# Performance work log

Measured on AMD Instinct MI355X. Metric: run time of the kernel, lower is better.

## Reference

```python
import jax, jax.numpy as jnp
import numpy as np

N, K, D = 32768, 1024, 256
TAU = 1.0          # gumbel-softmax temperature (torch default)
KL_WEIGHT = 1.0    # settings.kl_weight stand-in
EPS = 1e-6


def setup_inputs() -> dict:
    key = jax.random.key(0)
    k1, k2, k3 = jax.random.split(key, 3)
    latents = jax.random.normal(k1, (N, D), dtype=jnp.float32)
    # torch init: uniform_(-1/num_protos, 1/num_protos)
    prototypes = jax.random.uniform(k2, (K, D), dtype=jnp.float32,
                                    minval=-1.0 / K, maxval=1.0 / K)
    u = jax.random.uniform(k3, (N, K), dtype=jnp.float32,
                           minval=1e-10, maxval=1.0)
    gumbel = -jnp.log(-jnp.log(u))  # Gumbel(0,1) noise
    return {"latents": latents, "prototypes": prototypes, "gumbel": gumbel}


def reference(latents, prototypes, gumbel):
    # squared euclidean distances latents[:,None,:] - prototypes -> [N, K]
    # expanded form (same math, avoids [N,K,D] intermediate):
    d2 = (jnp.sum(latents * latents, axis=-1, keepdims=True)
          - 2.0 * latents @ prototypes.T
          + jnp.sum(prototypes * prototypes, axis=-1))
    logits = (-d2 + gumbel) / TAU
    logprobs = jax.nn.log_softmax(logits, axis=-1)      # [N, K]
    y_soft = jnp.exp(logprobs)
    # hard=True straight-through one-hot
    idx = jnp.argmax(y_soft, axis=-1)
    y_hard = jax.nn.one_hot(idx, K, dtype=y_soft.dtype)
    onehot = y_hard - jax.lax.stop_gradient(y_soft) + y_soft
    quantized = onehot @ prototypes                     # [N, D]

    # prior over codes (batch mean of probs), broadcast to all rows
    prior = jnp.mean(y_soft + EPS, axis=0)              # [K]
    # KLDivLoss(reduction='batchmean')(logprobs, prior):
    # mean over rows of sum_k prior_k * (log prior_k - logprobs_k)
    capacity = jnp.mean(jnp.sum(prior * (jnp.log(prior) - logprobs), axis=-1))
    ent = -jnp.sum(prior * jnp.log(prior))
    # settings.epoch <= 5000 branch: subtract entropy term
    vq_loss = KL_WEIGHT * capacity - 0.001 * ent
    return quantized, vq_loss
```

## Files before the change

### kernel.cpp

```cpp
#include <hip/hip_runtime.h>
#include <hip/hip_bf16.h>
#include <stdint.h>

#define NN 32768
#define KK 1024
#define DD 256
#define BM 16
#define CHUNK 128
#define NCHUNK (KK / CHUNK)
#define NTHR 512
#define NRB (NN / BM)

#define LXS 0
#define LPS 8192
#define ASC_MAXP 73728
#define ASC_ZP   74752
#define ASC_MI   75264
#define LA_TOT   75328

#define LSS 8192
#define LRM (LSS + 32768)
#define LRI (LRM + 64)
#define FLPS 41216
#define LTOT_PRE  41216
#define LTOT_NPRE (41216 + 65536)

#define PB_OFF   12288
#define SBUF_OFF 536576
#define LZ_OFF   (SBUF_OFF + (size_t)NRB * NCHUNK * 512 * 8)
#define WS_FULL  (LZ_OFF + (size_t)NN * 4)
#define WS_PRE   (PB_OFF + (size_t)KK * DD * 2)

typedef __attribute__((ext_vector_type(8))) short bf16x8;
typedef __attribute__((ext_vector_type(4))) float f32x4;

__device__ __forceinline__ uint32_t pkbf2(float a, float b) {
    uint32_t ua = __builtin_bit_cast(uint32_t, a);
    uint32_t ub = __builtin_bit_cast(uint32_t, b);
    ua = (ua + 0x7fffu + ((ua >> 16) & 1u)) >> 16;
    ub = (ub + 0x7fffu + ((ub >> 16) & 1u)) >> 16;
    return ua | (ub << 16);
}
__device__ __forceinline__ float ubf(uint32_t h) {
    return __builtin_bit_cast(float, h << 16);
}

__global__ void vq_init(const float* __restrict__ protos, float* __restrict__ ws) {
    int k = blockIdx.x * 256 + threadIdx.x;
    const float4* p4 = reinterpret_cast<const float4*>(protos + (size_t)k * DD);
    float s = 0.f;
#pragma unroll 8
    for (int j = 0; j < DD / 4; ++j) {
        float4 v = p4[j];
        s = fmaf(v.x, v.x, s); s = fmaf(v.y, v.y, s);
        s = fmaf(v.z, v.z, s); s = fmaf(v.w, v.w, s);
    }
    ws[k] = s;
    ws[KK + k] = 0.f;
    ws[2 * KK + k] = 0.f;
}

__global__ void vq_cvt(const float* __restrict__ protos, uint32_t* __restrict__ pb) {
    int idx = blockIdx.x * 256 + threadIdx.x;
    const float4* s = reinterpret_cast<const float4*>(protos + (size_t)idx * 8);
    float4 a = s[0], b = s[1];
    uint4 v;
    v.x = pkbf2(a.x, a.y); v.y = pkbf2(a.z, a.w);
    v.z = pkbf2(b.x, b.y); v.w = pkbf2(b.z, b.w);
    reinterpret_cast<uint4*>(pb)[idx] = v;
}

__global__ __launch_bounds__(NTHR) void vq_mainA(const float* __restrict__ latents,
                                                 const float* __restrict__ protos,
                                                 const float* __restrict__ gumbel,
                                                 float* __restrict__ ws,
                                                 float* __restrict__ out) {
    __shared__ __align__(16) unsigned char sm[LA_TOT];
    const int t = threadIdx.x;
    const int lane = t & 63;
    const int w = t >> 6;
    const int rb = blockIdx.x;
    const int n0 = rb * BM;
    const int l15 = lane & 15;
    const int l4 = lane >> 4;
    const float* np2 = ws;
    const uint4* pb = reinterpret_cast<const uint4*>((char*)ws + PB_OFF);
    uint2* Sb = reinterpret_cast<uint2*>((char*)ws + SBUF_OFF);
    float* lzb = reinterpret_cast<float*>((char*)ws + LZ_OFF);

    {
        int row = t >> 5, g = t & 31;
        const float4* src = reinterpret_cast<const float4*>(
            latents + (size_t)(n0 + row) * DD + g * 8);
        float4 a = src[0], b = src[1];
        uint4 v; v.x = pkbf2(a.x, a.y); v.y = pkbf2(a.z, a.w);
        v.z = pkbf2(b.x, b.y); v.w = pkbf2(b.z, b.w);
        *reinterpret_cast<uint4*>(sm + LXS + row * 512 + ((g ^ (row & 7)) << 4)) = v;
    }

    const int pr = w * 16 + l15;
    const int cwbase = w * 16 + l4 * 4;
    float z = 0.f, m = -3.4e38f; int mi = 0;

    for (int c = 0; c < NCHUNK; ++c) {
        __syncthreads();
#pragma unroll
        for (int i = 0; i < 8; ++i) {
            int G = t + NTHR * i;
            int p = G >> 5, g = G & 31;
            *reinterpret_cast<uint4*>(sm + LPS + p * 512 + ((g ^ (p & 7)) << 4)) =
                pb[(size_t)(c * CHUNK + p) * 32 + g];
        }
        __syncthreads();

        const int pg0 = c * CHUNK + cwbase;
        float4 q4 = *reinterpret_cast<const float4*>(np2 + pg0);
        float4 g4 = *reinterpret_cast<const float4*>(gumbel + (size_t)(n0 + l15) * KK + pg0);

        f32x4 acc = {0.f, 0.f, 0.f, 0.f};
#pragma unroll
        for (int ks = 0; ks < 8; ++ks) {
            int gi = ks * 4 + l4;
            bf16x8 af = *reinterpret_cast<bf16x8*>(sm + LPS + pr * 512 + ((gi ^ (pr & 7)) << 4));
            bf16x8 b0 = *reinterpret_cast<bf16x8*>(sm + LXS + l15 * 512 + ((gi ^ (l15 & 7)) << 4));
            acc = __builtin_amdgcn_mfma_f32_16x16x32_bf16(af, b0, acc, 0, 0, 0);
        }
        float s0 = fmaf(2.f, acc.x, -q4.x) + g4.x;
        float s1 = fmaf(2.f, acc.y, -q4.y) + g4.y;
        float s2 = fmaf(2.f, acc.z, -q4.z) + g4.z;
        float s3 = fmaf(2.f, acc.w, -q4.w) + g4.w;
        z += __expf(s0) + __expf(s1) + __expf(s2) + __expf(s3);
        if (s0 > m) { m = s0; mi = pg0; }
        if (s1 > m) { m = s1; mi = pg0 + 1; }
        if (s2 > m) { m = s2; mi = pg0 + 2; }
        if (s3 > m) { m = s3; mi = pg0 + 3; }
        uint2 pk;
        pk.x = pkbf2(s0, s1);
        pk.y = pkbf2(s2, s3);
        Sb[((size_t)rb * NCHUNK + c) * 512 + t] = pk;
    }

#pragma unroll
    for (int off = 16; off <= 32; off <<= 1) {
        float om = __shfl_xor(m, off); int oi = __shfl_xor(mi, off);
        if (om > m || (om == m && oi < mi)) { m = om; mi = oi; }
        z += __shfl_xor(z, off);
    }
    if (lane < 16) {
        *reinterpret_cast<float*>(sm + ASC_MAXP + (l15 * 8 + w) * 8) = m;
        *reinterpret_cast<int*>(sm + ASC_MAXP + (l15 * 8 + w) * 8 + 4) = mi;
        *reinterpret_cast<float*>(sm + ASC_ZP + (l15 * 8 + w) * 4) = z;
    }
    __syncthreads();
    if (t < 16) {
        float mm = -3.4e38f; int mmi = 0; float Z = 0.f;
#pragma unroll
        for (int j = 0; j < 8; ++j) {
            float om = *reinterpret_cast<float*>(sm + ASC_MAXP + (t * 8 + j) * 8);
            int oi = *reinterpret_cast<int*>(sm + ASC_MAXP + (t * 8 + j) * 8 + 4);
            if (om > mm || (om == mm && oi < mmi)) { mm = om; mmi = oi; }
            Z += *reinterpret_cast<float*>(sm + ASC_ZP + (t * 8 + j) * 4);
        }
        lzb[n0 + t] = __logf(Z);
        *reinterpret_cast<int*>(sm + ASC_MI + t * 4) = mmi;
    }
    __syncthreads();

    {
        int row = t >> 5, v = t & 31;
        int idx = *reinterpret_cast<int*>(sm + ASC_MI + row * 4);
        const float4* src = reinterpret_cast<const float4*>(protos + (size_t)idx * DD + v * 8);
        float4* dst = reinterpret_cast<float4*>(out + (size_t)(n0 + row) * DD + v * 8);
        dst[0] = src[0];
        dst[1] = src[1];
    }
}

__global__ __launch_bounds__(NTHR) void vq_colsum(float* __restrict__ ws) {
    const int t = threadIdx.x;
    const int l15 = t & 15;
    const int c = blockIdx.x & 7;
    const int rg = blockIdx.x >> 3;
    const uint2* Sb = reinterpret_cast<const uint2*>((char*)ws + SBUF_OFF);
    const float* lzb = reinterpret_cast<const float*>((char*)ws + LZ_OFF);
    float* colsum_y = ws + KK;
    float* colsum_lp = ws + 2 * KK;

    float sy0 = 0.f, sy1 = 0.f, sy2 = 0.f, sy3 = 0.f;
    float sl0 = 0.f, sl1 = 0.f, sl2 = 0.f, sl3 = 0.f;
    for (int i = 0; i < NRB / 32; ++i) {
        int rb = rg * (NRB / 32) + i;
        uint2 v = Sb[((size_t)rb * NCHUNK + c) * 512 + t];
        float lz = lzb[rb * BM + l15];
        float a0 = ubf(v.x & 0xffffu) - lz, a1 = ubf(v.x >> 16) - lz;
        float a2 = ubf(v.y & 0xffffu) - lz, a3 = ubf(v.y >> 16) - lz;
        sy0 += __expf(a0); sy1 += __expf(a1); sy2 += __expf(a2); sy3 += __expf(a3);
        sl0 += a0; sl1 += a1; sl2 += a2; sl3 += a3;
    }
#pragma unroll
    for (int off = 1; off < 16; off <<= 1) {
        sy0 += __shfl_xor(sy0, off); sy1 += __shfl_xor(sy1, off);
        sy2 += __shfl_xor(sy2, off); sy3 += __shfl_xor(sy3, off);
        sl0 += __shfl_xor(sl0, off); sl1 += __shfl_xor(sl1, off);
        sl2 += __shfl_xor(sl2, off); sl3 += __shfl_xor(sl3, off);
    }
    if (l15 == 0) {
        int w = t >> 6, l4 = (t & 63) >> 4;
        int cb = c * CHUNK + w * 16 + l4 * 4;
        atomicAdd(&colsum_y[cb],     sy0); atomicAdd(&colsum_y[cb + 1], sy1);
        atomicAdd(&colsum_y[cb + 2], sy2); atomicAdd(&colsum_y[cb + 3], sy3);
        atomicAdd(&colsum_lp[cb],     sl0); atomicAdd(&colsum_lp[cb + 1], sl1);
        atomicAdd(&colsum_lp[cb + 2], sl2); atomicAdd(&colsum_lp[cb + 3], sl3);
    }
}

template<bool PRE>
__global__ __launch_bounds__(NTHR) void vq_mainT(const float* __restrict__ latents,
                                                 const float* __restrict__ protos,
                                                 const float* __restrict__ gumbel,
                                                 float* __restrict__ ws,
                                                 float* __restrict__ out) {
    __shared__ __align__(16) unsigned char sm[PRE ? LTOT_PRE : LTOT_NPRE];
    const int t = threadIdx.x;
    const int lane = t & 63;
    const int w = t >> 6;
    const int n0 = blockIdx.x * BM;
    const int l15 = lane & 15;
    const int l4 = lane >> 4;
    const float* np2 = ws;
    float* colsum_y = ws + KK;
    float* colsum_lp = ws + 2 * KK;
    const uint4* pb = reinterpret_cast<const uint4*>((char*)ws + PB_OFF);

    {
        int row = t >> 5, g = t & 31;
        const float4* src = reinterpret_cast<const float4*>(
            latents + (size_t)(n0 + row) * DD + g * 8);
        float4 a = src[0], b = src[1];
        uint4 v; v.x = pkbf2(a.x, a.y); v.y = pkbf2(a.z, a.w);
        v.z = pkbf2(b.x, b.y); v.w = pkbf2(b.z, b.w);
        *reinterpret_cast<uint4*>(sm + LXS + row * 512 + ((g ^ (row & 7)) << 4)) = v;
    }
    __syncthreads();

    const int pr = w * 16 + l15;
    const int cwbase = w * 16 + l4 * 4;

    for (int c = 0; c < NCHUNK; ++c) {
        if (!PRE) {
            __syncthreads();
#pragma unroll
            for (int i = 0; i < 8; ++i) {
                int G = t + NTHR * i;
                int p = G >> 5, g = G & 31;
                const float4* src = reinterpret_cast<const float4*>(
                    protos + (size_t)(c * CHUNK + p) * DD + g * 8);
                float4 a = src[0], b = src[1];
                uint4 v; v.x = pkbf2(a.x, a.y); v.y = pkbf2(a.z, a.w);
                v.z = pkbf2(b.x, b.y); v.w = pkbf2(b.z, b.w);
                *reinterpret_cast<uint4*>(sm + FLPS + p * 512 + ((g ^ (p & 7)) << 4)) = v;
            }
            __syncthreads();
        }
        const int pg0 = c * CHUNK + cwbase;
        float4 q4 = *reinterpret_cast<const float4*>(np2 + pg0);
        float4 g4 = *reinterpret_cast<const float4*>(gumbel + (size_t)(n0 + l15) * KK + pg0);

        f32x4 acc = {0.f, 0.f, 0.f, 0.f};
        if (PRE) {
            const uint4* afp = pb + (size_t)(c * CHUNK + pr) * 32;
#pragma unroll
            for (int ks = 0; ks < 8; ++ks) {
                int gi = ks * 4 + l4;
                bf16x8 af = __builtin_bit_cast(bf16x8, afp[gi]);
                bf16x8 b0 = *reinterpret_cast<bf16x8*>(
                    sm + LXS + l15 * 512 + ((gi ^ (l15 & 7)) << 4));
                acc = __builtin_amdgcn_mfma_f32_16x16x32_bf16(af, b0, acc, 0, 0, 0);
            }
        } else {
#pragma unroll
            for (int ks = 0; ks < 8; ++ks) {
                int gi = ks * 4 + l4;
                bf16x8 af = *reinterpret_cast<bf16x8*>(
                    sm + FLPS + pr * 512 + ((gi ^ (pr & 7)) << 4));
                bf16x8 b0 = *reinterpret_cast<bf16x8*>(
                    sm + LXS + l15 * 512 + ((gi ^ (l15 & 7)) << 4));
                acc = __builtin_amdgcn_mfma_f32_16x16x32_bf16(af, b0, acc, 0, 0, 0);
            }
        }
        {
            const int Gs = pg0 >> 2;
            uint2 pk;
            pk.x = pkbf2(fmaf(2.f, acc.x, -q4.x) + g4.x, fmaf(2.f, acc.y, -q4.y) + g4.y);
            pk.y = pkbf2(fmaf(2.f, acc.z, -q4.z) + g4.z, fmaf(2.f, acc.w, -q4.w) + g4.w);
            *reinterpret_cast<uint2*>(sm + LSS + l15 * 2048 + ((Gs ^ ((l15 & 7) << 1)) << 3)) = pk;
        }
    }
    __syncthreads();

    {
        int row = t >> 5, v = t & 31;
        int sw = (row & 7) << 1;
        uint2 d[8];
#pragma unroll
        for (int j = 0; j < 8; ++j) {
            int G = v + 32 * j;
            d[j] = *reinterpret_cast<uint2*>(sm + LSS + row * 2048 + ((G ^ sw) << 3));
        }
        float m = -3.4e38f; int mi = 0;
#pragma unroll
        for (int j = 0; j < 8; ++j) {
            int c0 = (v + 32 * j) * 4;
            float f0 = ubf(d[j].x & 0xffffu), f1 = ubf(d[j].x >> 16);
            float f2 = ubf(d[j].y & 0xffffu), f3 = ubf(d[j].y >> 16);
            if (f0 > m) { m = f0; mi = c0; }
            if (f1 > m) { m = f1; mi = c0 + 1; }
            if (f2 > m) { m = f2; mi = c0 + 2; }
            if (f3 > m) { m = f3; mi = c0 + 3; }
        }
#pragma unroll
        for (int off = 1; off < 32; off <<= 1) {
            float om = __shfl_xor(m, off);
            int oi = __shfl_xor(mi, off);
            if (om > m || (om == m && oi < mi)) { m = om; mi = oi; }
        }
        float se = 0.f;
#pragma unroll
        for (int j = 0; j < 8; ++j) {
            se += __expf(ubf(d[j].x & 0xffffu) - m);
            se += __expf(ubf(d[j].x >> 16) - m);
            se += __expf(ubf(d[j].y & 0xffffu) - m);
            se += __expf(ubf(d[j].y >> 16) - m);
        }
#pragma unroll
        for (int off = 1; off < 32; off <<= 1) se += __shfl_xor(se, off);
        if (v == 0) {
            *reinterpret_cast<float*>(sm + LRM + row * 4) = m + __logf(se);
            *reinterpret_cast<int*>(sm + LRI + row * 4) = mi;
        }
    }
    __syncthreads();

#pragma unroll
    for (int h = 0; h < 2; ++h) {
        int col = t + h * NTHR;
        int G = col >> 2;
        int e2 = (col & 3) << 1;
        float sy = 0.f, slp = 0.f;
#pragma unroll 8
        for (int r = 0; r < BM; ++r) {
            uint32_t hv = *reinterpret_cast<uint16_t*>(
                sm + LSS + r * 2048 + ((G ^ ((r & 7) << 1)) << 3) + e2);
            float lz = *reinterpret_cast<float*>(sm + LRM + r * 4);
            float lp = ubf(hv) - lz;
            slp += lp;
            sy += __expf(lp);
        }
        atomicAdd(&colsum_y[col], sy);
        atomicAdd(&colsum_lp[col], slp);
    }

    {
        int row = t >> 5, v = t & 31;
        int idx = *reinterpret_cast<int*>(sm + LRI + row * 4);
        const float4* src = reinterpret_cast<const float4*>(protos + (size_t)idx * DD + v * 8);
        float4* dst = reinterpret_cast<float4*>(out + (size_t)(n0 + row) * DD + v * 8);
        dst[0] = src[0];
        dst[1] = src[1];
    }
}

__global__ void vq_final(const float* __restrict__ ws,
                         float* __restrict__ out, int out_size) {
    __shared__ float part[4];
    int t = threadIdx.x;
    const float invN = 1.0f / (float)NN;
    float a = 0.f;
    for (int j = 0; j < 4; ++j) {
        int k = t + j * 256;
        float prior = fmaf(ws[KK + k], invN, 1e-6f);
        float Lk = ws[2 * KK + k] * invN;
        a += prior * (1.001f * __logf(prior) - Lk);
    }
#pragma unroll
    for (int off = 32; off >= 1; off >>= 1) a += __shfl_xor(a, off);
    if ((t & 63) == 0) part[t >> 6] = a;
    __syncthreads();
    if (t == 0) {
        out[out_size - 1] = part[0] + part[1] + part[2] + part[3];
    }
}

extern "C" void kernel_launch(void* const* d_in, const int* in_sizes, int n_in,
                              void* d_out, int out_size, void* d_ws, size_t ws_size,
                              hipStream_t stream) {
    (void)in_sizes; (void)n_in;
    const float* latents = (const float*)d_in[0];
    const float* protos  = (const float*)d_in[1];
    const float* gumbel  = (const float*)d_in[2];
    float* out           = (float*)d_out;
    float* ws            = (float*)d_ws;

    vq_init<<<dim3(4), dim3(256), 0, stream>>>(protos, ws);
    if (ws_size >= WS_FULL) {
        vq_cvt<<<dim3(KK * DD / 2048), dim3(256), 0, stream>>>(
            protos, (uint32_t*)((char*)d_ws + PB_OFF));
        vq_mainA<<<dim3(NRB), dim3(NTHR), 0, stream>>>(
            latents, protos, gumbel, ws, out);
        vq_colsum<<<dim3(NCHUNK * 32), dim3(NTHR), 0, stream>>>(ws);
    } else if (ws_size >= WS_PRE) {
        vq_cvt<<<dim3(KK * DD / 2048), dim3(256), 0, stream>>>(
            protos, (uint32_t*)((char*)d_ws + PB_OFF));
        vq_mainT<true><<<dim3(NRB), dim3(NTHR), 0, stream>>>(
            latents, protos, gumbel, ws, out);
    } else {
        vq_mainT<false><<<dim3(NRB), dim3(NTHR), 0, stream>>>(
            latents, protos, gumbel, ws, out);
    }
    vq_final<<<dim3(1), dim3(256), 0, stream>>>(ws, out, out_size);
}
```

Before: 121.9 us.

## Retile main kernel to 32-row blocks with 64-prototype chunks

The main kernel now processes 32 latent rows per block instead of 16, and streams prototypes in 64-row chunks instead of 128. The 8 waves are split into 4 prototype column groups times 2 row halves. Each staged prototype tile is therefore reused across twice as many rows, which halves the total prototype traffic through LDS and shrinks LDS usage to allow more resident blocks. In exchange there are twice as many chunk iterations and barriers per block. The colsum reduction and the fallback kernel indexing are updated to match the new layout.

```diff
diff --git a/kernel.cpp b/kernel.cpp
--- a/kernel.cpp
+++ b/kernel.cpp
@@ -5,19 +5,20 @@
 #define NN 32768
 #define KK 1024
 #define DD 256
-#define BM 16
-#define CHUNK 128
+#define BM 32
+#define CHUNK 64
 #define NCHUNK (KK / CHUNK)
 #define NTHR 512
 #define NRB (NN / BM)
 
 #define LXS 0
-#define LPS 8192
-#define ASC_MAXP 73728
-#define ASC_ZP   74752
-#define ASC_MI   75264
-#define LA_TOT   75328
-
+#define LPS 16384
+#define LA_TOT 49152
+#define SC_MAXP 0
+#define SC_ZP   1024
+#define SC_MI   1536
+
+#define BMF 16
 #define LSS 8192
 #define LRM (LSS + 32768)
 #define LRI (LRM + 64)
@@ -83,29 +84,36 @@
     const int n0 = rb * BM;
     const int l15 = lane & 15;
     const int l4 = lane >> 4;
+    const int wq = w & 3;
+    const int wh = w >> 2;
+    const int xr = wh * 16 + l15;
     const float* np2 = ws;
     const uint4* pb = reinterpret_cast<const uint4*>((char*)ws + PB_OFF);
     uint2* Sb = reinterpret_cast<uint2*>((char*)ws + SBUF_OFF);
     float* lzb = reinterpret_cast<float*>((char*)ws + LZ_OFF);
 
     {
-        int row = t >> 5, g = t & 31;
-        const float4* src = reinterpret_cast<const float4*>(
-            latents + (size_t)(n0 + row) * DD + g * 8);
-        float4 a = src[0], b = src[1];
-        uint4 v; v.x = pkbf2(a.x, a.y); v.y = pkbf2(a.z, a.w);
-        v.z = pkbf2(b.x, b.y); v.w = pkbf2(b.z, b.w);
-        *reinterpret_cast<uint4*>(sm + LXS + row * 512 + ((g ^ (row & 7)) << 4)) = v;
-    }
-
-    const int pr = w * 16 + l15;
-    const int cwbase = w * 16 + l4 * 4;
+        int row = t >> 4;
+        int g0 = (t & 15) * 2;
+#pragma unroll
+        for (int j = 0; j < 2; ++j) {
+            int g = g0 + j;
+            const float4* src = reinterpret_cast<const float4*>(
+                latents + (size_t)(n0 + row) * DD + g * 8);
+            float4 a = src[0], b = src[1];
+            uint4 v; v.x = pkbf2(a.x, a.y); v.y = pkbf2(a.z, a.w);
+            v.z = pkbf2(b.x, b.y); v.w = pkbf2(b.z, b.w);
+            *reinterpret_cast<uint4*>(sm + LXS + row * 512 + ((g ^ (row & 7)) << 4)) = v;
+        }
+    }
+
+    const int pr = wq * 16 + l15;
     float z = 0.f, m = -3.4e38f; int mi = 0;
 
     for (int c = 0; c < NCHUNK; ++c) {
         __syncthreads();
 #pragma unroll
-        for (int i = 0; i < 8; ++i) {
+        for (int i = 0; i < 4; ++i) {
             int G = t + NTHR * i;
             int p = G >> 5, g = G & 31;
             *reinterpret_cast<uint4*>(sm + LPS + p * 512 + ((g ^ (p & 7)) << 4)) =
@@ -113,16 +121,16 @@
         }
         __syncthreads();
 
-        const int pg0 = c * CHUNK + cwbase;
+        const int pg0 = c * CHUNK + wq * 16 + l4 * 4;
         float4 q4 = *reinterpret_cast<const float4*>(np2 + pg0);
-        float4 g4 = *reinterpret_cast<const float4*>(gumbel + (size_t)(n0 + l15) * KK + pg0);
+        float4 g4 = *reinterpret_cast<const float4*>(gumbel + (size_t)(n0 + xr) * KK + pg0);
 
         f32x4 acc = {0.f, 0.f, 0.f, 0.f};
 #pragma unroll
         for (int ks = 0; ks < 8; ++ks) {
             int gi = ks * 4 + l4;
             bf16x8 af = *reinterpret_cast<bf16x8*>(sm + LPS + pr * 512 + ((gi ^ (pr & 7)) << 4));
-            bf16x8 b0 = *reinterpret_cast<bf16x8*>(sm + LXS + l15 * 512 + ((gi ^ (l15 & 7)) << 4));
+            bf16x8 b0 = *reinterpret_cast<bf16x8*>(sm + LXS + xr * 512 + ((gi ^ (xr & 7)) << 4));
             acc = __builtin_amdgcn_mfma_f32_16x16x32_bf16(af, b0, acc, 0, 0, 0);
         }
         float s0 = fmaf(2.f, acc.x, -q4.x) + g4.x;
@@ -134,11 +142,10 @@
         if (s1 > m) { m = s1; mi = pg0 + 1; }
         if (s2 > m) { m = s2; mi = pg0 + 2; }
         if (s3 > m) { m = s3; mi = pg0 + 3; }
-        uint2 pk;
-        pk.x = pkbf2(s0, s1);
-        pk.y = pkbf2(s2, s3);
+        uint2 pk; pk.x = pkbf2(s0, s1); pk.y = pkbf2(s2, s3);
         Sb[((size_t)rb * NCHUNK + c) * 512 + t] = pk;
     }
+    __syncthreads();
 
 #pragma unroll
     for (int off = 16; off <= 32; off <<= 1) {
@@ -147,51 +154,52 @@
         z += __shfl_xor(z, off);
     }
     if (lane < 16) {
-        *reinterpret_cast<float*>(sm + ASC_MAXP + (l15 * 8 + w) * 8) = m;
-        *reinterpret_cast<int*>(sm + ASC_MAXP + (l15 * 8 + w) * 8 + 4) = mi;
-        *reinterpret_cast<float*>(sm + ASC_ZP + (l15 * 8 + w) * 4) = z;
-    }
-    __syncthreads();
-    if (t < 16) {
+        *reinterpret_cast<float*>(sm + SC_MAXP + (xr * 4 + wq) * 8) = m;
+        *reinterpret_cast<int*>(sm + SC_MAXP + (xr * 4 + wq) * 8 + 4) = mi;
+        *reinterpret_cast<float*>(sm + SC_ZP + (xr * 4 + wq) * 4) = z;
+    }
+    __syncthreads();
+    if (t < 32) {
         float mm = -3.4e38f; int mmi = 0; float Z = 0.f;
 #pragma unroll
-        for (int j = 0; j < 8; ++j) {
-            float om = *reinterpret_cast<float*>(sm + ASC_MAXP + (t * 8 + j) * 8);
-            int oi = *reinterpret_cast<int*>(sm + ASC_MAXP + (t * 8 + j) * 8 + 4);
+        for (int j = 0; j < 4; ++j) {
+            float om = *reinterpret_cast<float*>(sm + SC_MAXP + (t * 4 + j) * 8);
+            int oi = *reinterpret_cast<int*>(sm + SC_MAXP + (t * 4 + j) * 8 + 4);
             if (om > mm || (om == mm && oi < mmi)) { mm = om; mmi = oi; }
-            Z += *reinterpret_cast<float*>(sm + ASC_ZP + (t * 8 + j) * 4);
+            Z += *reinterpret_cast<float*>(sm + SC_ZP + (t * 4 + j) * 4);
         }
         lzb[n0 + t] = __logf(Z);
-        *reinterpret_cast<int*>(sm + ASC_MI + t * 4) = mmi;
+        *reinterpret_cast<int*>(sm + SC_MI + t * 4) = mmi;
     }
     __syncthreads();
 
     {
-        int row = t >> 5, v = t & 31;
-        int idx = *reinterpret_cast<int*>(sm + ASC_MI + row * 4);
-        const float4* src = reinterpret_cast<const float4*>(protos + (size_t)idx * DD + v * 8);
-        float4* dst = reinterpret_cast<float4*>(out + (size_t)(n0 + row) * DD + v * 8);
-        dst[0] = src[0];
-        dst[1] = src[1];
+        int row = t >> 4, v = t & 15;
+        int idx = *reinterpret_cast<int*>(sm + SC_MI + row * 4);
+        const float4* src = reinterpret_cast<const float4*>(protos + (size_t)idx * DD + v * 16);
+        float4* dst = reinterpret_cast<float4*>(out + (size_t)(n0 + row) * DD + v * 16);
+#pragma unroll
+        for (int j = 0; j < 4; ++j) dst[j] = src[j];
     }
 }
 
 __global__ __launch_bounds__(NTHR) void vq_colsum(float* __restrict__ ws) {
     const int t = threadIdx.x;
     const int l15 = t & 15;
-    const int c = blockIdx.x & 7;
-    const int rg = blockIdx.x >> 3;
+    const int c = blockIdx.x & 15;
+    const int rg = blockIdx.x >> 4;
     const uint2* Sb = reinterpret_cast<const uint2*>((char*)ws + SBUF_OFF);
     const float* lzb = reinterpret_cast<const float*>((char*)ws + LZ_OFF);
     float* colsum_y = ws + KK;
     float* colsum_lp = ws + 2 * KK;
+    const int xr = ((t >> 8) & 1) * 16 + l15;
 
     float sy0 = 0.f, sy1 = 0.f, sy2 = 0.f, sy3 = 0.f;
     float sl0 = 0.f, sl1 = 0.f, sl2 = 0.f, sl3 = 0.f;
     for (int i = 0; i < NRB / 32; ++i) {
         int rb = rg * (NRB / 32) + i;
         uint2 v = Sb[((size_t)rb * NCHUNK + c) * 512 + t];
-        float lz = lzb[rb * BM + l15];
+        float lz = lzb[rb * BM + xr];
         float a0 = ubf(v.x & 0xffffu) - lz, a1 = ubf(v.x >> 16) - lz;
         float a2 = ubf(v.y & 0xffffu) - lz, a3 = ubf(v.y >> 16) - lz;
         sy0 += __expf(a0); sy1 += __expf(a1); sy2 += __expf(a2); sy3 += __expf(a3);
@@ -205,8 +213,7 @@
         sl2 += __shfl_xor(sl2, off); sl3 += __shfl_xor(sl3, off);
     }
     if (l15 == 0) {
-        int w = t >> 6, l4 = (t & 63) >> 4;
-        int cb = c * CHUNK + w * 16 + l4 * 4;
+        int cb = c * CHUNK + ((t >> 6) & 3) * 16 + ((t >> 4) & 3) * 4;
         atomicAdd(&colsum_y[cb],     sy0); atomicAdd(&colsum_y[cb + 1], sy1);
         atomicAdd(&colsum_y[cb + 2], sy2); atomicAdd(&colsum_y[cb + 3], sy3);
         atomicAdd(&colsum_lp[cb],     sl0); atomicAdd(&colsum_lp[cb + 1], sl1);
@@ -224,7 +231,7 @@
     const int t = threadIdx.x;
     const int lane = t & 63;
     const int w = t >> 6;
-    const int n0 = blockIdx.x * BM;
+    const int n0 = blockIdx.x * BMF;
     const int l15 = lane & 15;
     const int l4 = lane >> 4;
     const float* np2 = ws;
@@ -239,14 +246,14 @@
         float4 a = src[0], b = src[1];
         uint4 v; v.x = pkbf2(a.x, a.y); v.y = pkbf2(a.z, a.w);
         v.z = pkbf2(b.x, b.y); v.w = pkbf2(b.z, b.w);
-        *reinterpret_cast<uint4*>(sm + LXS + row * 512 + ((g ^ (row & 7)) << 4)) = v;
+        *reinterpret_cast<uint4*>(sm + row * 512 + ((g ^ (row & 7)) << 4)) = v;
     }
     __syncthreads();
 
     const int pr = w * 16 + l15;
     const int cwbase = w * 16 + l4 * 4;
 
-    for (int c = 0; c < NCHUNK; ++c) {
+    for (int c = 0; c < 8; ++c) {
         if (!PRE) {
             __syncthreads();
 #pragma unroll
@@ -254,7 +261,7 @@
                 int G = t + NTHR * i;
                 int p = G >> 5, g = G & 31;
                 const float4* src = reinterpret_cast<const float4*>(
-                    protos + (size_t)(c * CHUNK + p) * DD + g * 8);
+                    protos + (size_t)(c * 128 + p) * DD + g * 8);
                 float4 a = src[0], b = src[1];
                 uint4 v; v.x = pkbf2(a.x, a.y); v.y = pkbf2(a.z, a.w);
                 v.z = pkbf2(b.x, b.y); v.w = pkbf2(b.z, b.w);
@@ -262,19 +269,19 @@
             }
             __syncthreads();
         }
-        const int pg0 = c * CHUNK + cwbase;
+        const int pg0 = c * 128 + cwbase;
         float4 q4 = *reinterpret_cast<const float4*>(np2 + pg0);
         float4 g4 = *reinterpret_cast<const float4*>(gumbel + (size_t)(n0 + l15) * KK + pg0);
 
         f32x4 acc = {0.f, 0.f, 0.f, 0.f};
         if (PRE) {
-            const uint4* afp = pb + (size_t)(c * CHUNK + pr) * 32;
+            const uint4* afp = pb + (size_t)(c * 128 + pr) * 32;
 #pragma unroll
             for (int ks = 0; ks < 8; ++ks) {
                 int gi = ks * 4 + l4;
                 bf16x8 af = __builtin_bit_cast(bf16x8, afp[gi]);
                 bf16x8 b0 = *reinterpret_cast<bf16x8*>(
-                    sm + LXS + l15 * 512 + ((gi ^ (l15 & 7)) << 4));
+                    sm + l15 * 512 + ((gi ^ (l15 & 7)) << 4));
                 acc = __builtin_amdgcn_mfma_f32_16x16x32_bf16(af, b0, acc, 0, 0, 0);
             }
         } else {
@@ -284,7 +291,7 @@
                 bf16x8 af = *reinterpret_cast<bf16x8*>(
                     sm + FLPS + pr * 512 + ((gi ^ (pr & 7)) << 4));
                 bf16x8 b0 = *reinterpret_cast<bf16x8*>(
-                    sm + LXS + l15 * 512 + ((gi ^ (l15 & 7)) << 4));
+                    sm + l15 * 512 + ((gi ^ (l15 & 7)) << 4));
                 acc = __builtin_amdgcn_mfma_f32_16x16x32_bf16(af, b0, acc, 0, 0, 0);
             }
         }
@@ -348,7 +355,7 @@
         int e2 = (col & 3) << 1;
         float sy = 0.f, slp = 0.f;
 #pragma unroll 8
-        for (int r = 0; r < BM; ++r) {
+        for (int r = 0; r < BMF; ++r) {
             uint32_t hv = *reinterpret_cast<uint16_t*>(
                 sm + LSS + r * 2048 + ((G ^ ((r & 7) << 1)) << 3) + e2);
             float lz = *reinterpret_cast<float*>(sm + LRM + r * 4);
@@ -411,10 +418,10 @@
     } else if (ws_size >= WS_PRE) {
         vq_cvt<<<dim3(KK * DD / 2048), dim3(256), 0, stream>>>(
             protos, (uint32_t*)((char*)d_ws + PB_OFF));
-        vq_mainT<true><<<dim3(NRB), dim3(NTHR), 0, stream>>>(
+        vq_mainT<true><<<dim3(NN / BMF), dim3(NTHR), 0, stream>>>(
             latents, protos, gumbel, ws, out);
     } else {
-        vq_mainT<false><<<dim3(NRB), dim3(NTHR), 0, stream>>>(
+        vq_mainT<false><<<dim3(NN / BMF), dim3(NTHR), 0, stream>>>(
             latents, protos, gumbel, ws, out);
     }
     vq_final<<<dim3(1), dim3(256), 0, stream>>>(ws, out, out_size);
```

New measurement: 134.1 us. 10.0% more time.
